# Performance work log

Measured on AMD Instinct MI355X. Metric: run time of the kernel, lower is better.

## Reference

```python
import jax, jax.numpy as jnp
import numpy as np

B, Z, K, T = 4, 64, 400, 48000
CIN, COUT, KS, DIL = 128, 128, 3, 1
H = 32


def setup_inputs() -> dict:
    key = jax.random.key(0)
    ks = jax.random.split(key, 10)
    s = lambda n: 1.0 / np.sqrt(n)
    return {
        "x": jax.random.normal(ks[0], (B, CIN, T), jnp.float32),
        "z": jax.random.normal(ks[1], (B, Z, K), jnp.float32),
        # weight_model: Conv1d(Z->H, k=1), ReLU, Conv1d(H -> CIN*COUT*KS, k=1)
        "w1": jax.random.normal(ks[2], (H, Z), jnp.float32) * s(Z),
        "b1": jax.random.normal(ks[3], (H,), jnp.float32) * 0.01,
        "w2": jax.random.normal(ks[4], (CIN * COUT * KS, H), jnp.float32) * s(H),
        "b2": jax.random.normal(ks[5], (CIN * COUT * KS,), jnp.float32) * s(CIN * KS),
        # bias_model: Conv1d(Z->H, k=1), ReLU, Conv1d(H -> COUT, k=1)
        "bw1": jax.random.normal(ks[6], (H, Z), jnp.float32) * s(Z),
        "bb1": jax.random.normal(ks[7], (H,), jnp.float32) * 0.01,
        "bw2": jax.random.normal(ks[8], (COUT, H), jnp.float32) * s(H),
        "bb2": jax.random.normal(ks[9], (COUT,), jnp.float32) * 0.01,
    }


def _mlp1x1(z, wa, ba, wb, bb):
    # two pointwise Conv1d layers with ReLU in between; z: [B, Z, K]
    h = jax.nn.relu(jnp.einsum('hz,bzk->bhk', wa, z) + ba[None, :, None])
    return jnp.einsum('oh,bhk->bok', wb, h) + bb[None, :, None]


def _unfold_causal(x, ksize, dil):
    # causal im2col: tap i is x delayed by i*dil samples (left-padded with zeros)
    pad = dil * (ksize - 1)
    xp = jnp.pad(x, ((0, 0), (0, 0), (pad, 0)))
    taps = [xp[:, :, pad - i * dil: pad - i * dil + x.shape[-1]] for i in range(ksize)]
    return jnp.concatenate(taps, axis=1)  # [B, CIN*KS, T]


def reference(x, z, w1, b1, w2, b2, bw1, bb1, bw2, bb2):
    Tk = T // K  # samples per weight chunk
    xu = _unfold_causal(x, KS, DIL)                       # [B, CIN*KS, T]
    xr = xu.transpose(0, 2, 1).reshape(B * K, Tk, CIN * KS)
    w = _mlp1x1(z, w1, b1, w2, b2)                        # [B, CIN*COUT*KS, K]
    w = w.reshape(B, CIN * KS, COUT, K).transpose(0, 3, 1, 2).reshape(B * K, CIN * KS, COUT)
    bias = _mlp1x1(z, bw1, bb1, bw2, bb2)                 # [B, COUT, K]
    bias = bias.transpose(0, 2, 1).reshape(B * K, COUT)
    y = jnp.einsum('btc,bco->bto', xr, w) + bias[:, None, :]
    return y.reshape(B, T, COUT).transpose(0, 2, 1)       # [B, COUT, T]
```

## Files before the change

kernel.cpp:

```cpp
#include <hip/hip_runtime.h>
#include <stdint.h>

#define TT     48000
#define TK     120
#define NC     128
#define NA     384
#define NZ     64
#define NH     32
#define NK     400
#define NCHUNK 1600
#define MW     49152
#define XROWS  48002

typedef float f32x4 __attribute__((ext_vector_type(4)));
typedef __bf16 bf16x8 __attribute__((ext_vector_type(8)));

static __device__ __forceinline__ uint16_t f2bf(float f) {
    uint32_t x; __builtin_memcpy(&x, &f, 4);
    return (uint16_t)((x + 0x7fffu + ((x >> 16) & 1u)) >> 16);
}

__global__ __launch_bounds__(256) void k0x(
    const float* __restrict__ x, uint16_t* __restrict__ Xt) {
    int t0 = blockIdx.x * 128, cin0 = blockIdx.y * 64, b = blockIdx.z;
    int tid = threadIdx.x;
    __shared__ __align__(16) uint16_t Lt[128][72];
    const float* xb = x + ((size_t)b * NC + cin0) * TT + t0;
    int cg = (tid & 7) * 8;
    int tq = (tid >> 3) * 4;
    uint16_t vb[4][8];
#pragma unroll
    for (int i = 0; i < 8; ++i) {
        float4 v = *(const float4*)(xb + (size_t)(cg + i) * TT + tq);
        vb[0][i] = f2bf(v.x); vb[1][i] = f2bf(v.y);
        vb[2][i] = f2bf(v.z); vb[3][i] = f2bf(v.w);
    }
#pragma unroll
    for (int j = 0; j < 4; ++j) {
        uint4 o; __builtin_memcpy(&o, vb[j], 16);
        *(uint4*)&Lt[tq + j][cg] = o;
    }
    __syncthreads();
    uint16_t* XtB = Xt + (size_t)b * XROWS * NC;
#pragma unroll
    for (int r = 0; r < 4; ++r) {
        int s = r * 256 + tid;
        int t = s >> 3, cc = s & 7;
        uint4 o = *(uint4*)&Lt[t][cc * 8];
        *(uint4*)(XtB + (size_t)(t0 + t + 2) * NC + cin0 + cc * 8) = o;
    }
    if (blockIdx.x == 0 && blockIdx.y == 0 && tid < 32)
        *(uint4*)(XtB + tid * 8) = make_uint4(0, 0, 0, 0);
}

__global__ __launch_bounds__(256) void k1_hidden(
    const float* __restrict__ z,
    const float* __restrict__ w1, const float* __restrict__ b1,
    const float* __restrict__ bw1, const float* __restrict__ bb1,
    const float* __restrict__ bw2, const float* __restrict__ bb2,
    uint16_t* __restrict__ Hb, float* __restrict__ biasws) {
    int tid = threadIdx.x, lane = tid & 63, w = tid >> 6;
    int chunk0 = blockIdx.x * 4;
    int b = chunk0 / NK;
    int k0 = chunk0 - b * NK;

    __shared__ float w1sT[64][33];
    __shared__ float bw1sT[64][33];
    __shared__ float bw2s[128][33];
    __shared__ float zs[64][4];
    __shared__ float hbs[4][33];
    __shared__ float b1s[32], bb1s[32], bb2s[128];

    {
        int row = tid >> 3, c0 = (tid & 7) * 8;
        float4 a0 = *(const float4*)(w1 + row * NZ + c0);
        float4 a1 = *(const float4*)(w1 + row * NZ + c0 + 4);
        float4 c0v = *(const float4*)(bw1 + row * NZ + c0);
        float4 c1v = *(const float4*)(bw1 + row * NZ + c0 + 4);
        const float av[8] = {a0.x,a0.y,a0.z,a0.w,a1.x,a1.y,a1.z,a1.w};
        const float cv[8] = {c0v.x,c0v.y,c0v.z,c0v.w,c1v.x,c1v.y,c1v.z,c1v.w};
#pragma unroll
        for (int j = 0; j < 8; ++j) {
            w1sT[c0 + j][row]  = av[j];
            bw1sT[c0 + j][row] = cv[j];
        }
    }
    {
        int r = tid >> 1, cb = (tid & 1) * 16;
        float4 v0 = *(const float4*)(bw2 + r * NH + cb);
        float4 v1 = *(const float4*)(bw2 + r * NH + cb + 4);
        float4 v2 = *(const float4*)(bw2 + r * NH + cb + 8);
        float4 v3 = *(const float4*)(bw2 + r * NH + cb + 12);
        const float vv[16] = {v0.x,v0.y,v0.z,v0.w,v1.x,v1.y,v1.z,v1.w,
                              v2.x,v2.y,v2.z,v2.w,v3.x,v3.y,v3.z,v3.w};
#pragma unroll
        for (int j = 0; j < 16; ++j) bw2s[r][cb + j] = vv[j];
    }
    if (tid < 64) {
        float4 zv = *(const float4*)(z + ((size_t)b * NZ + tid) * NK + k0);
        zs[tid][0] = zv.x; zs[tid][1] = zv.y; zs[tid][2] = zv.z; zs[tid][3] = zv.w;
    }
    if (tid < 32) { b1s[tid] = b1[tid]; bb1s[tid] = bb1[tid]; }
    if (tid >= 128 && tid < 256) bb2s[tid - 128] = bb2[tid - 128];
    __syncthreads();

    int chunk = chunk0 + w;
    if (lane < NH) {
        float s = b1s[lane];
#pragma unroll
        for (int i = 0; i < NZ; ++i) s = fmaf(w1sT[i][lane], zs[i][w], s);
        Hb[(size_t)chunk * NH + lane] = f2bf(fmaxf(s, 0.f));
    } else {
        int j = lane - NH;
        float s = bb1s[j];
#pragma unroll
        for (int i = 0; i < NZ; ++i) s = fmaf(bw1sT[i][j], zs[i][w], s);
        hbs[w][j] = fmaxf(s, 0.f);
    }

#pragma unroll
    for (int r = 0; r < 2; ++r) {
        int c = r * 64 + lane;
        float s = bb2s[c];
#pragma unroll
        for (int j = 0; j < NH; ++j) s = fmaf(bw2s[c][j], hbs[w][j], s);
        biasws[(size_t)chunk * NC + c] = s;
    }
}

__global__ __launch_bounds__(256) void k2_wgen(
    const float* __restrict__ w2, const float* __restrict__ b2,
    const uint16_t* __restrict__ Hb, uint16_t* __restrict__ Wt,
    int chunk0, int nchunk) {
    int tid = threadIdx.x, lane = tid & 63, w = tid >> 6;
    int quad = lane >> 4, li = lane & 15;
    __shared__ __align__(16) uint16_t St[4][16][68];
    int mb = blockIdx.x * 256 + w * 64;

    bf16x8 afrag[4];
    float4 bias[4];
#pragma unroll
    for (int t = 0; t < 4; ++t) {
        int mp = mb + t * 16 + li;
        int a = mp % NA, c = mp / NA;
        const float* src = w2 + ((size_t)a * NC + c) * NH + quad * 8;
        float4 v0 = *(const float4*)(src);
        float4 v1 = *(const float4*)(src + 4);
        uint16_t tmp[8] = { f2bf(v0.x), f2bf(v0.y), f2bf(v0.z), f2bf(v0.w),
                            f2bf(v1.x), f2bf(v1.y), f2bf(v1.z), f2bf(v1.w) };
        __builtin_memcpy(&afrag[t], tmp, 16);
        float bv[4];
#pragma unroll
        for (int r = 0; r < 4; ++r) {
            int mpr = mb + t * 16 + quad * 4 + r;
            bv[r] = b2[(size_t)(mpr % NA) * NC + (mpr / NA)];
        }
        bias[t] = make_float4(bv[0], bv[1], bv[2], bv[3]);
    }

    for (int g = 0; g < 10; ++g) {
        int cl0 = blockIdx.y * 160 + g * 16;
        if (cl0 >= nchunk) break;
        int cl = cl0 + li;
        if (cl >= nchunk) cl = nchunk - 1;
        bf16x8 hfrag = *(const bf16x8*)(Hb + (size_t)(chunk0 + cl) * NH + quad * 8);
#pragma unroll
        for (int t = 0; t < 4; ++t) {
            f32x4 acc = {0.f, 0.f, 0.f, 0.f};
            acc = __builtin_amdgcn_mfma_f32_16x16x32_bf16(afrag[t], hfrag, acc, 0, 0, 0);
            uint16_t p[4] = { f2bf(acc[0] + bias[t].x), f2bf(acc[1] + bias[t].y),
                              f2bf(acc[2] + bias[t].z), f2bf(acc[3] + bias[t].w) };
            uint64_t pv; __builtin_memcpy(&pv, p, 8);
            *(uint64_t*)&St[w][li][t * 16 + quad * 4] = pv;
        }
#pragma unroll
        for (int p = 0; p < 2; ++p) {
            int ch = (lane >> 3) + p * 8, part = lane & 7;
            uint4 v = *(const uint4*)&St[w][ch][part * 8];
            int cg = cl0 + ch;
            if (cg < nchunk)
                *(uint4*)(Wt + (size_t)cg * MW + mb + part * 8) = v;
        }
    }
}

__global__ __launch_bounds__(512) void k3_conv(
    const uint16_t* __restrict__ Xt, const uint16_t* __restrict__ Wt,
    const float* __restrict__ biasws, float* __restrict__ out, int chunk0) {
    int cl = blockIdx.x, chunk = chunk0 + cl;
    int b = chunk / NK, k = chunk - b * NK;
    int kbase = k * TK;
    int tid = threadIdx.x, lane = tid & 63, w = tid >> 6;
    int quad = lane >> 4, li = lane & 15;
    int tblk = (w >> 1) * 32, cblk = (w & 1) * 64;

    __shared__ __align__(16) char smem[81920];
    char* Xa  = smem;
    char* Db0 = smem + 32768;
    char* Db1 = smem + 49152;
    char* Db2 = smem + 65536;
    const uint16_t* XtB = Xt + (size_t)b * XROWS * NC;
    const uint16_t* WtC = Wt + (size_t)cl * MW;

    f32x4 acc[2][4];
#pragma unroll
    for (int i = 0; i < 2; ++i)
#pragma unroll
        for (int j = 0; j < 4; ++j) acc[i][j] = (f32x4){0.f, 0.f, 0.f, 0.f};

    auto stageD = [&](char* dst, int dks) {
#pragma unroll
        for (int j = 0; j < 2; ++j) {
            int g = (w * 2 + j) * 64 + lane;
            int c = g >> 3, sd = g & 7;
            int o = sd ^ (c & 7);
            const uint16_t* gsrc = WtC + (size_t)c * NA + dks * 64 + o * 8;
            __builtin_amdgcn_global_load_lds(
                (__attribute__((address_space(1))) void*)gsrc,
                (__attribute__((address_space(3))) void*)(dst + (w * 2 + j) * 1024),
                16, 0, 0);
        }
    };

#pragma unroll
    for (int i = 0; i < 4; ++i) {
        int brow = w * 16 + i * 4 + quad;
        const uint16_t* g = XtB + (size_t)(kbase + brow) * NC
                          + ((li ^ (brow & 15)) * 8);
        __builtin_amdgcn_global_load_lds(
            (__attribute__((address_space(1))) void*)g,
            (__attribute__((address_space(3))) void*)(Xa + (w * 16 + i * 4) * 256),
            16, 0, 0);
    }
    stageD(Db0, 0);
    stageD(Db1, 1);

#pragma unroll
    for (int dk = 0; dk < 6; ++dk) {
        if (dk < 5) asm volatile("s_waitcnt vmcnt(2)" ::: "memory");
        else        asm volatile("s_waitcnt vmcnt(0)" ::: "memory");
        __builtin_amdgcn_s_barrier();
        __builtin_amdgcn_sched_barrier(0);
        if (dk < 4) {
            int sel = (dk + 2) % 3;
            stageD(sel == 0 ? Db0 : (sel == 1 ? Db1 : Db2), dk + 2);
        }
        int cs = dk % 3;
        char* cur = cs == 0 ? Db0 : (cs == 1 ? Db1 : Db2);
        int tap = dk >> 1;

        bf16x8 bfr[2][4];
#pragma unroll
        for (int s = 0; s < 2; ++s)
#pragma unroll
            for (int ct = 0; ct < 4; ++ct) {
                int c = cblk + ct * 16 + li;
                bfr[s][ct] = *(const bf16x8*)(cur + c * 128
                             + (((s * 4 + quad) ^ (c & 7)) << 4));
            }
#pragma unroll
        for (int s = 0; s < 2; ++s) {
            bf16x8 af[2];
#pragma unroll
            for (int tt = 0; tt < 2; ++tt) {
                int r = tblk + tt * 16 + li + 2 - tap;
                r = r > 127 ? 127 : r;
                int q = (dk & 1) * 8 + s * 4 + quad;
                af[tt] = *(const bf16x8*)(Xa + r * 256 + ((q ^ (r & 15)) << 4));
            }
#pragma unroll
            for (int tt = 0; tt < 2; ++tt)
#pragma unroll
                for (int ct = 0; ct < 4; ++ct)
                    acc[tt][ct] = __builtin_amdgcn_mfma_f32_16x16x32_bf16(
                        af[tt], bfr[s][ct], acc[tt][ct], 0, 0, 0);
        }
    }

#pragma unroll
    for (int ct = 0; ct < 4; ++ct) {
        int c = cblk + ct * 16 + li;
        float bias = biasws[(size_t)chunk * NC + c];
        float* ob = out + ((size_t)b * NC + c) * TT + kbase;
#pragma unroll
        for (int tt = 0; tt < 2; ++tt) {
            int t0v = tblk + tt * 16 + quad * 4;
            if (t0v < TK) {
                f32x4 v = acc[tt][ct];
                *(float4*)(ob + t0v) = make_float4(v[0] + bias, v[1] + bias,
                                                   v[2] + bias, v[3] + bias);
            }
        }
    }
}

extern "C" void kernel_launch(void* const* d_in, const int* in_sizes, int n_in,
                              void* d_out, int out_size, void* d_ws, size_t ws_size,
                              hipStream_t stream) {
    const float* x   = (const float*)d_in[0];
    const float* z   = (const float*)d_in[1];
    const float* w1  = (const float*)d_in[2];
    const float* b1  = (const float*)d_in[3];
    const float* w2  = (const float*)d_in[4];
    const float* b2  = (const float*)d_in[5];
    const float* bw1 = (const float*)d_in[6];
    const float* bb1 = (const float*)d_in[7];
    const float* bw2 = (const float*)d_in[8];
    const float* bb2 = (const float*)d_in[9];
    float* out = (float*)d_out;

    char* ws = (char*)d_ws;
    uint16_t* Hb     = (uint16_t*)(ws);
    float*    biasws = (float*)(ws + 102400);
    uint16_t* Xt     = (uint16_t*)(ws + 921600);
    const size_t wt_off = 50079744;
    uint16_t* Wt     = (uint16_t*)(ws + wt_off);

    size_t avail = (ws_size > wt_off) ? (ws_size - wt_off) : 0;
    int batch = (int)(avail / ((size_t)MW * 2));
    if (batch > 800) batch = 800;
    if (batch < 1) batch = 1;

    k0x<<<dim3(TT / 128, 2, 4), 256, 0, stream>>>(x, Xt);
    k1_hidden<<<NCHUNK / 4, 256, 0, stream>>>(z, w1, b1, bw1, bb1, bw2, bb2, Hb, biasws);

    for (int c0 = 0; c0 < NCHUNK; c0 += batch) {
        int nc = NCHUNK - c0;
        if (nc > batch) nc = batch;
        dim3 g2(MW / 256, (nc + 159) / 160, 1);
        k2_wgen<<<g2, 256, 0, stream>>>(w2, b2, Hb, Wt, c0, nc);
        k3_conv<<<nc, 512, 0, stream>>>(Xt, Wt, biasws, out, c0);
    }
}
```

Before: 291.2 us.

## Fuse x transpose/bf16 conversion into conv kernel, drop k0x pre-pass

Removes the separate k0x kernel that transposed x into a bf16 time-major workspace buffer. The conv kernel now loads fp32 x directly, converts it to bf16, packs pairs of channels and writes them into swizzled LDS, including the two causal halo rows. This avoids a full write and re-read of a roughly 49MB intermediate and one launch. In exchange each conv block does its own strided fp32 loads and conversion instead of an async global-to-LDS copy. The launch bound gains an occupancy hint and the workspace offset for Wt shrinks.

After: 284.6 us, median of 2. 2.3% less time.

```diff
diff --git a/kernel.cpp b/kernel.cpp
--- a/kernel.cpp
+++ b/kernel.cpp
@@ -10,7 +10,6 @@
 #define NK     400
 #define NCHUNK 1600
 #define MW     49152
-#define XROWS  48002
 
 typedef float f32x4 __attribute__((ext_vector_type(4)));
 typedef __bf16 bf16x8 __attribute__((ext_vector_type(8)));
@@ -19,38 +18,8 @@
     uint32_t x; __builtin_memcpy(&x, &f, 4);
     return (uint16_t)((x + 0x7fffu + ((x >> 16) & 1u)) >> 16);
 }
-
-__global__ __launch_bounds__(256) void k0x(
-    const float* __restrict__ x, uint16_t* __restrict__ Xt) {
-    int t0 = blockIdx.x * 128, cin0 = blockIdx.y * 64, b = blockIdx.z;
-    int tid = threadIdx.x;
-    __shared__ __align__(16) uint16_t Lt[128][72];
-    const float* xb = x + ((size_t)b * NC + cin0) * TT + t0;
-    int cg = (tid & 7) * 8;
-    int tq = (tid >> 3) * 4;
-    uint16_t vb[4][8];
-#pragma unroll
-    for (int i = 0; i < 8; ++i) {
-        float4 v = *(const float4*)(xb + (size_t)(cg + i) * TT + tq);
-        vb[0][i] = f2bf(v.x); vb[1][i] = f2bf(v.y);
-        vb[2][i] = f2bf(v.z); vb[3][i] = f2bf(v.w);
-    }
-#pragma unroll
-    for (int j = 0; j < 4; ++j) {
-        uint4 o; __builtin_memcpy(&o, vb[j], 16);
-        *(uint4*)&Lt[tq + j][cg] = o;
-    }
-    __syncthreads();
-    uint16_t* XtB = Xt + (size_t)b * XROWS * NC;
-#pragma unroll
-    for (int r = 0; r < 4; ++r) {
-        int s = r * 256 + tid;
-        int t = s >> 3, cc = s & 7;
-        uint4 o = *(uint4*)&Lt[t][cc * 8];
-        *(uint4*)(XtB + (size_t)(t0 + t + 2) * NC + cin0 + cc * 8) = o;
-    }
-    if (blockIdx.x == 0 && blockIdx.y == 0 && tid < 32)
-        *(uint4*)(XtB + tid * 8) = make_uint4(0, 0, 0, 0);
+static __device__ __forceinline__ uint32_t pk2u(uint16_t lo, uint16_t hi) {
+    return (uint32_t)lo | ((uint32_t)hi << 16);
 }
 
 __global__ __launch_bounds__(256) void k1_hidden(
@@ -184,8 +153,8 @@
     }
 }
 
-__global__ __launch_bounds__(512) void k3_conv(
-    const uint16_t* __restrict__ Xt, const uint16_t* __restrict__ Wt,
+__global__ __launch_bounds__(512, 4) void k3_conv(
+    const float* __restrict__ x, const uint16_t* __restrict__ Wt,
     const float* __restrict__ biasws, float* __restrict__ out, int chunk0) {
     int cl = blockIdx.x, chunk = chunk0 + cl;
     int b = chunk / NK, k = chunk - b * NK;
@@ -199,14 +168,7 @@
     char* Db0 = smem + 32768;
     char* Db1 = smem + 49152;
     char* Db2 = smem + 65536;
-    const uint16_t* XtB = Xt + (size_t)b * XROWS * NC;
     const uint16_t* WtC = Wt + (size_t)cl * MW;
-
-    f32x4 acc[2][4];
-#pragma unroll
-    for (int i = 0; i < 2; ++i)
-#pragma unroll
-        for (int j = 0; j < 4; ++j) acc[i][j] = (f32x4){0.f, 0.f, 0.f, 0.f};
 
     auto stageD = [&](char* dst, int dks) {
 #pragma unroll
@@ -222,18 +184,52 @@
         }
     };
 
-#pragma unroll
-    for (int i = 0; i < 4; ++i) {
-        int brow = w * 16 + i * 4 + quad;
-        const uint16_t* g = XtB + (size_t)(kbase + brow) * NC
-                          + ((li ^ (brow & 15)) * 8);
-        __builtin_amdgcn_global_load_lds(
-            (__attribute__((address_space(1))) void*)g,
-            (__attribute__((address_space(3))) void*)(Xa + (w * 16 + i * 4) * 256),
-            16, 0, 0);
-    }
     stageD(Db0, 0);
     stageD(Db1, 1);
+
+    const float* xb = x + (size_t)b * NC * TT;
+    {
+        int thalf = lane >> 5;
+        int tq4 = (lane & 31) * 4;
+#pragma unroll
+        for (int i = 0; i < 4; ++i) {
+            int p = i * 16 + w * 2 + thalf;
+            int cin = p * 2;
+            int tg = kbase + tq4;
+            int tga = tg > TT - 4 ? TT - 4 : tg;
+            float4 v0 = *(const float4*)(xb + (size_t)cin * TT + tga);
+            float4 v1 = *(const float4*)(xb + (size_t)(cin + 1) * TT + tga);
+            uint32_t pks[4] = { pk2u(f2bf(v0.x), f2bf(v1.x)),
+                                pk2u(f2bf(v0.y), f2bf(v1.y)),
+                                pk2u(f2bf(v0.z), f2bf(v1.z)),
+                                pk2u(f2bf(v0.w), f2bf(v1.w)) };
+            int q = cin >> 3, wi = (cin & 7) * 2;
+#pragma unroll
+            for (int j = 0; j < 4; ++j) {
+                int r = tq4 + 2 + j;
+                if (r < 128)
+                    *(uint32_t*)(Xa + r * 256 + ((q ^ (r & 15)) << 4) + wi) = pks[j];
+            }
+            if (tq4 == 0) {
+                uint32_t r0 = 0, r1 = 0;
+                if (kbase > 0) {
+                    float2 u0 = *(const float2*)(xb + (size_t)cin * TT + kbase - 2);
+                    float2 u1 = *(const float2*)(xb + (size_t)(cin + 1) * TT + kbase - 2);
+                    r0 = pk2u(f2bf(u0.x), f2bf(u1.x));
+                    r1 = pk2u(f2bf(u0.y), f2bf(u1.y));
+                }
+                *(uint32_t*)(Xa + (q << 4) + wi) = r0;
+                *(uint32_t*)(Xa + 256 + ((q ^ 1) << 4) + wi) = r1;
+            }
+        }
+    }
+    asm volatile("s_waitcnt lgkmcnt(0)" ::: "memory");
+
+    f32x4 acc[2][4];
+#pragma unroll
+    for (int i = 0; i < 2; ++i)
+#pragma unroll
+        for (int j = 0; j < 4; ++j) acc[i][j] = (f32x4){0.f, 0.f, 0.f, 0.f};
 
 #pragma unroll
     for (int dk = 0; dk < 6; ++dk) {
@@ -312,8 +308,7 @@
     char* ws = (char*)d_ws;
     uint16_t* Hb     = (uint16_t*)(ws);
     float*    biasws = (float*)(ws + 102400);
-    uint16_t* Xt     = (uint16_t*)(ws + 921600);
-    const size_t wt_off = 50079744;
+    const size_t wt_off = 921600;
     uint16_t* Wt     = (uint16_t*)(ws + wt_off);
 
     size_t avail = (ws_size > wt_off) ? (ws_size - wt_off) : 0;
@@ -321,7 +316,6 @@
     if (batch > 800) batch = 800;
     if (batch < 1) batch = 1;
 
-    k0x<<<dim3(TT / 128, 2, 4), 256, 0, stream>>>(x, Xt);
     k1_hidden<<<NCHUNK / 4, 256, 0, stream>>>(z, w1, b1, bw1, bb1, bw2, bb2, Hb, biasws);
 
     for (int c0 = 0; c0 < NCHUNK; c0 += batch) {
@@ -329,6 +323,6 @@
         if (nc > batch) nc = batch;
         dim3 g2(MW / 256, (nc + 159) / 160, 1);
         k2_wgen<<<g2, 256, 0, stream>>>(w2, b2, Hb, Wt, c0, nc);
-        k3_conv<<<nc, 512, 0, stream>>>(Xt, Wt, biasws, out, c0);
-    }
-}
+        k3_conv<<<nc, 512, 0, stream>>>(x, Wt, biasws, out, c0);
+    }
+}
```
